# Kernel tuning notes

Hardware: AMD Instinct MI355X
Metric: run time of the kernel (lower is better)

## Reference

```python
import jax, jax.numpy as jnp
import numpy as np

N_HEAD = 16
D_MODEL = 1024
HEAD_DIM = D_MODEL // N_HEAD  # 64
LAMBDA_INIT = 0.8 - 0.6 * float(np.exp(-0.3 * 1))  # layer_depth = 1


def setup_inputs() -> dict:
    key = jax.random.key(0)
    ks = jax.random.split(key, 10)
    B, T, D = 1, 2048, D_MODEL
    std = 0.02
    return {
        "x": jax.random.normal(ks[0], (B, T, D), jnp.float32),
        "Wq": jax.random.normal(ks[1], (D, D), jnp.float32) * std,
        "Wk": jax.random.normal(ks[2], (D, D), jnp.float32) * std,
        "Wv": jax.random.normal(ks[3], (D, D), jnp.float32) * std,
        "Wproj": jax.random.normal(ks[4], (D, D), jnp.float32) * std,
        "lambda_q1": jax.random.normal(ks[5], (HEAD_DIM // 2,), jnp.float32) * 0.1,
        "lambda_k1": jax.random.normal(ks[6], (HEAD_DIM // 2,), jnp.float32) * 0.1,
        "lambda_q2": jax.random.normal(ks[7], (HEAD_DIM // 2,), jnp.float32) * 0.1,
        "lambda_k2": jax.random.normal(ks[8], (HEAD_DIM // 2,), jnp.float32) * 0.1,
    }


def _rms_norm(x):
    # F.rms_norm with no weight: x / sqrt(mean(x^2) + eps)
    eps = jnp.finfo(x.dtype).eps
    return x * jax.lax.rsqrt(jnp.mean(jnp.square(x), axis=-1, keepdims=True) + eps)


def _rotary_cos_sin(T, dim, base=10000.0):
    inv_freq = 1.0 / (base ** (jnp.arange(0, dim, 2, dtype=jnp.float32) / dim))
    freqs = jnp.outer(jnp.arange(T, dtype=jnp.float32), inv_freq)  # [T, dim/2]
    return jnp.cos(freqs), jnp.sin(freqs)


def _apply_rotary(x, cos, sin):
    # x: [B, T, 2, H, hd]; cos/sin: [T, hd/2] broadcast over (group, head)
    d = x.shape[-1] // 2
    c = cos[None, :, None, None, :]
    s = sin[None, :, None, None, :]
    x1, x2 = x[..., :d], x[..., d:]
    return jnp.concatenate([x1 * c + x2 * s, -x1 * s + x2 * c], axis=-1)


def _causal_attn(q, k, v, scale):
    # q,k: [B, T, H, hd]; v: [B, T, H, dv] -> [B, T, H, dv]
    T = q.shape[1]
    scores = jnp.einsum("bthd,bshd->bhts", q, k) * scale  # [B,H,T,T]
    mask = jnp.tril(jnp.ones((T, T), dtype=bool))
    scores = jnp.where(mask, scores, -jnp.inf)
    w = jax.nn.softmax(scores, axis=-1)
    return jnp.einsum("bhts,bshd->bthd", w, v)


def reference(x, Wq, Wk, Wv, Wproj, lambda_q1, lambda_k1, lambda_q2, lambda_k2):
    B, T, D = x.shape
    nh, hd = N_HEAD, HEAD_DIM
    q = (x @ Wq.T).reshape(B, T, 2, nh // 2, hd)
    k = (x @ Wk.T).reshape(B, T, 2, nh // 2, hd)
    v = (x @ Wv.T).reshape(B, T, nh // 2, 2 * hd)

    q, k = _rms_norm(q), _rms_norm(k)
    cos, sin = _rotary_cos_sin(T, hd)
    q, k = _apply_rotary(q, cos, sin), _apply_rotary(k, cos, sin)

    q1, q2 = q[:, :, 0], q[:, :, 1]
    k1, k2 = k[:, :, 0], k[:, :, 1]

    scale = 1.0 / jnp.sqrt(jnp.asarray(hd, x.dtype))
    y1 = _causal_attn(q1, k1, v, scale)  # [B,T,nh/2,2*hd]
    y2 = _causal_attn(q2, k2, v, scale)

    lambda_1 = jnp.exp(jnp.sum(lambda_q1 * lambda_k1))
    lambda_2 = jnp.exp(jnp.sum(lambda_q2 * lambda_k2))
    lambda_full = lambda_1 - lambda_2 + LAMBDA_INIT

    y = (y1 - lambda_full * y2).reshape(B, T, D)
    return y @ Wproj.T
```

## Files before the change

kernel.cpp:

```cpp
#include <hip/hip_runtime.h>
#include <hip/hip_bf16.h>

typedef __attribute__((ext_vector_type(4))) float f32x4;
typedef __attribute__((ext_vector_type(8))) short bf16x8;
typedef unsigned short u16;
typedef unsigned int u32;

#define T_SEQ 2048
#define DMODEL 1024

__device__ __forceinline__ u16 f2bf(float f) {
    __hip_bfloat16 h = __float2bfloat16(f);
    return __builtin_bit_cast(unsigned short, h);
}
__device__ __forceinline__ u16 f2h(float f) {
    _Float16 h = (_Float16)f;
    return __builtin_bit_cast(unsigned short, h);
}
__device__ __forceinline__ float h2f(u16 b) {
    return (float)__builtin_bit_cast(_Float16, b);
}

typedef const void __attribute__((address_space(1))) gvoid_t;
typedef void __attribute__((address_space(3))) lvoid_t;
__device__ __forceinline__ void gload16(const void* g, void* l) {
    __builtin_amdgcn_global_load_lds((gvoid_t*)g, (lvoid_t*)l, 16, 0, 0);
}

__device__ __forceinline__ void cast4(const float* __restrict__ s,
                                      u16* __restrict__ d, int u) {
    int i = u * 4;
    float4 v = *(const float4*)(s + i);
    ushort4 o;
    o.x = f2bf(v.x); o.y = f2bf(v.y); o.z = f2bf(v.z); o.w = f2bf(v.w);
    *(ushort4*)(d + i) = o;
}

__global__ __launch_bounds__(256) void prep(const float* __restrict__ x,
                                            const float* __restrict__ Wq,
                                            const float* __restrict__ Wk,
                                            const float* __restrict__ Wv,
                                            const float* __restrict__ Wp,
                                            u16* __restrict__ x_bf, u16* __restrict__ wq_bf,
                                            u16* __restrict__ wk_bf, u16* __restrict__ wv_bf,
                                            u16* __restrict__ wp_bf,
                                            float* __restrict__ cosT, float* __restrict__ sinT,
                                            const float* __restrict__ lq1, const float* __restrict__ lk1,
                                            const float* __restrict__ lq2, const float* __restrict__ lk2,
                                            float* __restrict__ lam) {
    int b = blockIdx.x;
    if (b < 6144) {
        int u = b * 256 + threadIdx.x;
        if (u < 524288)       cast4(x,  x_bf,  u);
        else if (u < 786432)  cast4(Wq, wq_bf, u - 524288);
        else if (u < 1048576) cast4(Wk, wk_bf, u - 786432);
        else if (u < 1310720) cast4(Wv, wv_bf, u - 1048576);
        else                  cast4(Wp, wp_bf, u - 1310720);
    } else if (b < 6400) {
        int i = (b - 6144) * 256 + threadIdx.x;
        int t = i >> 5, j = i & 31;
        float inv = powf(10000.0f, -(float)j * (1.0f / 32.0f));
        float fr = (float)t * inv;
        cosT[i] = cosf(fr);
        sinT[i] = sinf(fr);
    } else if (threadIdx.x == 0) {
        float s1 = 0.f, s2 = 0.f;
        for (int i = 0; i < 32; ++i) { s1 += lq1[i] * lk1[i]; s2 += lq2[i] * lk2[i]; }
        *lam = expf(s1) - expf(s2) + 0.35550906759096928f;
    }
}

__device__ __forceinline__ void gemm_main64(const u16* __restrict__ A,
                                            const u16* __restrict__ B,
                                            int m0, int n0, int K,
                                            u16* lA, u16* lB, f32x4 acc[2][4]) {
    const int tid = threadIdx.x;
    const int lane = tid & 63;
    const int wid = tid >> 6;
    const int wr = (wid >> 1) * 32;
    const int wc = (wid & 1) * 64;
    const int fr = lane & 15;
    const int kc = lane >> 4;
    const char* Ab = (const char*)A;
    const char* Bb = (const char*)B;
    const int rowbytes = K * 2;

    for (int k0 = 0; k0 < K; k0 += 64) {
#pragma unroll
        for (int i = 0; i < 2; ++i) {
            int seg = i * 256 + tid;
            int row = seg >> 3, cb = (seg & 7) * 16;
            gload16(Ab + (size_t)(m0 + row) * rowbytes + k0 * 2 + (cb ^ ((row & 7) << 4)),
                    (char*)lA + seg * 16);
        }
#pragma unroll
        for (int i = 0; i < 4; ++i) {
            int seg = i * 256 + tid;
            int row = seg >> 3, cb = (seg & 7) * 16;
            gload16(Bb + (size_t)(n0 + row) * rowbytes + k0 * 2 + (cb ^ ((row & 7) << 4)),
                    (char*)lB + seg * 16);
        }
        __syncthreads();
        bf16x8 a[2][2], b[4][2];
#pragma unroll
        for (int m = 0; m < 2; ++m)
#pragma unroll
            for (int kh = 0; kh < 2; ++kh) {
                int row = wr + m * 16 + fr;
                a[m][kh] = *(const bf16x8*)((char*)lA + row * 128 +
                                            ((kh * 64 + kc * 16) ^ ((row & 7) << 4)));
            }
#pragma unroll
        for (int n = 0; n < 4; ++n)
#pragma unroll
            for (int kh = 0; kh < 2; ++kh) {
                int row = wc + n * 16 + fr;
                b[n][kh] = *(const bf16x8*)((char*)lB + row * 128 +
                                            ((kh * 64 + kc * 16) ^ ((row & 7) << 4)));
            }
#pragma unroll
        for (int m = 0; m < 2; ++m)
#pragma unroll
            for (int n = 0; n < 4; ++n)
#pragma unroll
                for (int kh = 0; kh < 2; ++kh)
                    acc[m][n] = __builtin_amdgcn_mfma_f32_16x16x32_bf16(a[m][kh], b[n][kh],
                                                                        acc[m][n], 0, 0, 0);
        __syncthreads();
    }
}

__global__ __launch_bounds__(256) void gemm_qkv(const u16* __restrict__ A,
                                                const u16* __restrict__ wq,
                                                const u16* __restrict__ wk,
                                                const u16* __restrict__ wv,
                                                const float* __restrict__ cosT,
                                                const float* __restrict__ sinT,
                                                u16* __restrict__ q_bf,
                                                u16* __restrict__ k_bf,
                                                u16* __restrict__ vT) {
    __shared__ __align__(16) u16 lA[64 * 64];
    __shared__ __align__(16) u16 lB[128 * 64];
    const int nt = blockIdx.x;
    const int which = nt >> 3;
    const u16* B = (which == 0) ? wq : (which == 1) ? wk : wv;
    const int m0 = blockIdx.y * 64;
    const int n0 = (nt & 7) * 128;

    f32x4 acc[2][4] = {};
    gemm_main64(A, B, m0, n0, 1024, lA, lB, acc);

    const int lane = threadIdx.x & 63;
    const int wid = threadIdx.x >> 6;
    const int wr = (wid >> 1) * 32;
    const int wc = (wid & 1) * 64;
    const int fr = lane & 15;
    const int rr = (lane >> 4) * 4;

    if (which == 2) {
#pragma unroll
        for (int m = 0; m < 2; ++m) {
            int t0 = m0 + wr + m * 16 + rr;
#pragma unroll
            for (int n = 0; n < 4; ++n) {
                int cb = n0 + wc + n * 16 + fr;
                ushort4 w;
                w.x = f2bf(acc[m][n][0]);
                w.y = f2bf(acc[m][n][1]);
                w.z = f2bf(acc[m][n][2]);
                w.w = f2bf(acc[m][n][3]);
                *(ushort4*)(vT + (size_t)cb * T_SEQ + t0) = w;
            }
        }
        return;
    }

    const float oscale = (which == 0) ? 0.18033688011112042f : 1.0f;
    const int cb = n0 + wc;
    const int plane = ((cb >> 9) << 3) | ((cb >> 6) & 7);
    u16* dstp = ((which == 0) ? q_bf : k_bf) + (size_t)plane * T_SEQ * 64;
#pragma unroll
    for (int m = 0; m < 2; ++m)
#pragma unroll
        for (int r = 0; r < 4; ++r) {
            int t = m0 + wr + m * 16 + rr + r;
            float s2 = 0.f;
#pragma unroll
            for (int n = 0; n < 4; ++n) { float a = acc[m][n][r]; s2 += a * a; }
            s2 += __shfl_xor(s2, 1); s2 += __shfl_xor(s2, 2);
            s2 += __shfl_xor(s2, 4); s2 += __shfl_xor(s2, 8);
            float inv = rsqrtf(s2 * (1.0f / 64.0f) + 1.1920929e-7f);
#pragma unroll
            for (int n = 0; n < 4; ++n) {
                float a = acc[m][n][r] * inv;
                float p_ = acc[m][n ^ 2][r] * inv;
                int jj = ((n & 1) << 4) + fr;
                float c = cosT[t * 32 + jj], sn = sinT[t * 32 + jj];
                float ov = (n < 2) ? (a * c + p_ * sn) : (a * c - p_ * sn);
                dstp[(size_t)t * 64 + n * 16 + fr] = f2bf(ov * oscale);
            }
        }
}

__global__ __launch_bounds__(256) void gemm_proj(const u16* __restrict__ A,
                                                 const u16* __restrict__ B,
                                                 float* __restrict__ C) {
    __shared__ __align__(16) u16 lA[64 * 64];
    __shared__ __align__(16) u16 lB[128 * 64];
    const int m0 = blockIdx.y * 64;
    const int n0 = blockIdx.x * 128;
    f32x4 acc[2][4] = {};
    gemm_main64(A, B, m0, n0, 1024, lA, lB, acc);
    const int lane = threadIdx.x & 63;
    const int wid = threadIdx.x >> 6;
    const int wr = (wid >> 1) * 32;
    const int wc = (wid & 1) * 64;
    const int fr = lane & 15;
    const int rr = (lane >> 4) * 4;
#pragma unroll
    for (int m = 0; m < 2; ++m)
#pragma unroll
        for (int n = 0; n < 4; ++n)
#pragma unroll
            for (int r = 0; r < 4; ++r)
                C[(size_t)(m0 + wr + m * 16 + rr + r) * 1024 + (n0 + wc + n * 16 + fr)] =
                    acc[m][n][r];
}

__global__ __launch_bounds__(256, 6) void attn_kernel(const u16* __restrict__ q_bf,
                                                      const u16* __restrict__ k_bf,
                                                      const u16* __restrict__ vT_bf,
                                                      u16* __restrict__ Oc,
                                                      float2* __restrict__ ml) {
    __shared__ __align__(16) u16 lK[2][32 * 64];
    __shared__ __align__(16) u16 lV[2][64 * 64];

    const int tid = threadIdx.x, lane = tid & 63, wid = tid >> 6;
    const int bid = blockIdx.x;
    const int plane = bid & 15;
    const int u = bid >> 4;
    int qt, chunk;
    if (u < 32)      { qt = 31 - (u >> 2);              chunk = u & 3; }
    else if (u < 56) { int w = u - 32; qt = 23 - w / 3; chunk = w % 3; }
    else if (u < 72) { int w = u - 56; qt = 15 - (w >> 1); chunk = w & 1; }
    else             { qt = 7 - (u - 72);               chunk = 0; }
    const int ntot = 2 * qt + 2;
    const int tb = chunk * 16;
    const int te = min(tb + 16, ntot);
    const int q0 = qt * 64;
    const int h = plane & 7;

    const u16* qp = q_bf + (size_t)plane * T_SEQ * 64;
    const char* kp = (const char*)(k_bf + (size_t)plane * T_SEQ * 64);
    const char* vp = (const char*)(vT_bf + (size_t)h * 128 * T_SEQ);
    const int fr = lane & 15, kc = lane >> 4;
    const int qrow = q0 + wid * 16 + fr;

    bf16x8 aq[2];
#pragma unroll
    for (int kq = 0; kq < 2; ++kq)
        aq[kq] = *(const bf16x8*)(qp + (size_t)qrow * 64 + kq * 32 + kc * 8);

    f32x4 o[8] = {};
    float mi_l = -1e30f, li_l = 0.f;
    const int srcA = fr + ((kc & 1) << 5);
    const int srcB = srcA + 16;
    const bool hi = kc >= 2;

    auto stage = [&](int b, int t) {
        int s0 = t << 5;
        {
            int row = tid >> 3, cp = (tid & 7) * 16;
            gload16(kp + (size_t)(s0 + row) * 128 + (cp ^ ((row & 7) << 4)),
                    (char*)lK[b] + tid * 16);
        }
#pragma unroll
        for (int i = 0; i < 2; ++i) {
            int c = i * 256 + tid;
            int row = c >> 3, cb = (c & 7) * 16;
            int cbs = cb ^ ((row & 7) << 4);
            int d = row * 2 + (cbs >> 6);
            int kk = (cbs & 63) >> 1;
            gload16(vp + (size_t)d * (T_SEQ * 2) + (size_t)(s0 + kk) * 2,
                    (char*)lV[b] + c * 16);
        }
    };

    auto compute = [&](const char* lKb, const char* lVb, int s0, bool diag) {
        f32x4 sacc[2] = {};
        __builtin_amdgcn_s_setprio(1);
#pragma unroll
        for (int kq = 0; kq < 2; ++kq)
#pragma unroll
            for (int n = 0; n < 2; ++n) {
                int row = n * 16 + fr;
                bf16x8 bk = *(const bf16x8*)(lKb + row * 128 +
                                             ((kq * 64 + kc * 16) ^ ((row & 7) << 4)));
                sacc[n] = __builtin_amdgcn_mfma_f32_16x16x32_bf16(bk, aq[kq], sacc[n], 0, 0, 0);
            }
        __builtin_amdgcn_s_setprio(0);

        if (diag) {
#pragma unroll
            for (int n = 0; n < 2; ++n)
#pragma unroll
                for (int r = 0; r < 4; ++r)
                    if (s0 + n * 16 + kc * 4 + r > qrow) sacc[n][r] = -1e30f;
        }
        float rmax = -1e30f;
#pragma unroll
        for (int n = 0; n < 2; ++n)
#pragma unroll
            for (int r = 0; r < 4; ++r)
                rmax = fmaxf(rmax, sacc[n][r]);
        rmax = fmaxf(rmax, __shfl_xor(rmax, 16));
        rmax = fmaxf(rmax, __shfl_xor(rmax, 32));

        bool raise = rmax > mi_l + 8.0f;
        float f = raise ? __builtin_exp2f(mi_l - rmax) : 1.0f;
        if (raise) mi_l = rmax;

        float rs = 0.f;
#pragma unroll
        for (int n = 0; n < 2; ++n)
#pragma unroll
            for (int r = 0; r < 4; ++r) {
                float p = __builtin_exp2f(sacc[n][r] - mi_l);
                sacc[n][r] = p;
                rs += p;
            }
        rs += __shfl_xor(rs, 16);
        rs += __shfl_xor(rs, 32);
        li_l = li_l * f + rs;

        if (__any(raise)) {
#pragma unroll
            for (int n8 = 0; n8 < 8; ++n8)
#pragma unroll
                for (int r = 0; r < 4; ++r) o[n8][r] *= f;
        }

        u32 w32[2][2];
#pragma unroll
        for (int n = 0; n < 2; ++n)
#pragma unroll
            for (int w = 0; w < 2; ++w) {
                u32 rpk;
                asm("v_cvt_pk_bf16_f32 %0, %1, %2"
                    : "=v"(rpk) : "v"(sacc[n][2 * w]), "v"(sacc[n][2 * w + 1]));
                w32[n][w] = rpk;
            }

        u32 a0 = (u32)__shfl((int)w32[0][0], srcA);
        u32 a1 = (u32)__shfl((int)w32[0][1], srcA);
        u32 a2 = (u32)__shfl((int)w32[0][0], srcB);
        u32 a3 = (u32)__shfl((int)w32[0][1], srcB);
        u32 b0 = (u32)__shfl((int)w32[1][0], srcA);
        u32 b1 = (u32)__shfl((int)w32[1][1], srcA);
        u32 b2 = (u32)__shfl((int)w32[1][0], srcB);
        u32 b3 = (u32)__shfl((int)w32[1][1], srcB);
        union { u32 u4[4]; bf16x8 v; } ap;
        ap.u4[0] = hi ? b0 : a0;
        ap.u4[1] = hi ? b1 : a1;
        ap.u4[2] = hi ? b2 : a2;
        ap.u4[3] = hi ? b3 : a3;

        __builtin_amdgcn_s_setprio(1);
#pragma unroll
        for (int n8 = 0; n8 < 8; ++n8) {
            int d = n8 * 16 + fr;
            int row = d >> 1;
            int colb = (d & 1) * 64 + kc * 16;
            bf16x8 bv = *(const bf16x8*)(lVb + row * 128 + (colb ^ ((row & 7) << 4)));
            o[n8] = __builtin_amdgcn_mfma_f32_16x16x32_bf16(bv, ap.v, o[n8], 0, 0, 0);
        }
        __builtin_amdgcn_s_setprio(0);
    };

    stage(0, tb);
    for (int t = tb; t < te; ++t) {
        int ib = (t - tb) & 1;
        if (t + 1 < te) {
            stage(ib ^ 1, t + 1);
            asm volatile("s_waitcnt vmcnt(3)" ::: "memory");
        } else {
            asm volatile("s_waitcnt vmcnt(0)" ::: "memory");
        }
        __builtin_amdgcn_sched_barrier(0);
        __builtin_amdgcn_s_barrier();
        __builtin_amdgcn_sched_barrier(0);
        compute((const char*)lK[ib], (const char*)lV[ib], t << 5, t >= ntot - 2);
        __builtin_amdgcn_s_barrier();
    }

    const float inv_l = 1.0f / li_l;
    u16* Ob = Oc + ((size_t)(plane * 4 + chunk) * T_SEQ + qrow) * 128;
#pragma unroll
    for (int n8 = 0; n8 < 8; ++n8) {
        ushort4 w;
        w.x = f2h(o[n8][0] * inv_l);
        w.y = f2h(o[n8][1] * inv_l);
        w.z = f2h(o[n8][2] * inv_l);
        w.w = f2h(o[n8][3] * inv_l);
        *(ushort4*)(Ob + n8 * 16 + kc * 4) = w;
    }
    if (kc == 0)
        ml[(size_t)(plane * 4 + chunk) * T_SEQ + qrow] = make_float2(mi_l, li_l);
}

__global__ __launch_bounds__(256) void merge_kernel(const u16* __restrict__ Oc,
                                                    const float2* __restrict__ ml,
                                                    const float* __restrict__ lamp,
                                                    u16* __restrict__ yc) {
    int uu = blockIdx.x * 256 + threadIdx.x;
    int t = uu >> 8, rem = uu & 255, h = rem >> 5, d4 = (rem & 31) * 4;
    int qt = t >> 6;
    int nc = (qt + 8) >> 3;
    float lamv = *lamp;
    float yv[2][4];
#pragma unroll
    for (int v = 0; v < 2; ++v) {
        int plane = v * 8 + h;
        float2 m_l[4];
        float M = -1e30f;
#pragma unroll
        for (int c = 0; c < 4; ++c)
            if (c < nc) {
                m_l[c] = ml[(size_t)(plane * 4 + c) * T_SEQ + t];
                M = fmaxf(M, m_l[c].x);
            }
        float den = 0.f, a0 = 0.f, a1 = 0.f, a2 = 0.f, a3 = 0.f;
#pragma unroll
        for (int c = 0; c < 4; ++c)
            if (c < nc) {
                float w = __builtin_exp2f(m_l[c].x - M) * m_l[c].y;
                den += w;
                ushort4 ov = *(const ushort4*)(Oc +
                    ((size_t)(plane * 4 + c) * T_SEQ + t) * 128 + d4);
                a0 += w * h2f(ov.x);
                a1 += w * h2f(ov.y);
                a2 += w * h2f(ov.z);
                a3 += w * h2f(ov.w);
            }
        float inv = 1.0f / den;
        yv[v][0] = a0 * inv; yv[v][1] = a1 * inv;
        yv[v][2] = a2 * inv; yv[v][3] = a3 * inv;
    }
    ushort4 o;
    o.x = f2bf(yv[0][0] - lamv * yv[1][0]);
    o.y = f2bf(yv[0][1] - lamv * yv[1][1]);
    o.z = f2bf(yv[0][2] - lamv * yv[1][2]);
    o.w = f2bf(yv[0][3] - lamv * yv[1][3]);
    *(ushort4*)(yc + (size_t)t * 1024 + h * 128 + d4) = o;
}

extern "C" void kernel_launch(void* const* d_in, const int* in_sizes, int n_in,
                              void* d_out, int out_size, void* d_ws, size_t ws_size,
                              hipStream_t stream) {
    const float* x   = (const float*)d_in[0];
    const float* Wq  = (const float*)d_in[1];
    const float* Wk  = (const float*)d_in[2];
    const float* Wv  = (const float*)d_in[3];
    const float* Wp  = (const float*)d_in[4];
    const float* lq1 = (const float*)d_in[5];
    const float* lk1 = (const float*)d_in[6];
    const float* lq2 = (const float*)d_in[7];
    const float* lk2 = (const float*)d_in[8];
    float* out = (float*)d_out;

    char* ws = (char*)d_ws;
    u16*    x_bf  = (u16*)(ws);
    u16*    wq_bf = (u16*)(ws + (4ull << 20));
    u16*    wk_bf = (u16*)(ws + (6ull << 20));
    u16*    wv_bf = (u16*)(ws + (8ull << 20));
    u16*    wp_bf = (u16*)(ws + (10ull << 20));
    u16*    vT_bf = (u16*)(ws + (12ull << 20));
    u16*    q_bf  = (u16*)(ws + (16ull << 20));
    u16*    k_bf  = (u16*)(ws + (20ull << 20));
    u16*    Oc    = (u16*)(ws + (24ull << 20));
    float2* ml    = (float2*)(ws + (56ull << 20));
    u16*    yc_bf = (u16*)(ws + (57ull << 20));
    float*  cosT  = (float*)(ws + (61ull << 20));
    float*  sinT  = (float*)(ws + (61ull << 20) + (256ull << 10));
    float*  lam   = (float*)(ws + (61ull << 20) + (512ull << 10));

    prep<<<6401, 256, 0, stream>>>(x, Wq, Wk, Wv, Wp,
                                   x_bf, wq_bf, wk_bf, wv_bf, wp_bf,
                                   cosT, sinT, lq1, lk1, lq2, lk2, lam);

    gemm_qkv<<<dim3(24, 32), 256, 0, stream>>>(x_bf, wq_bf, wk_bf, wv_bf,
                                               cosT, sinT, q_bf, k_bf, vT_bf);

    attn_kernel<<<1280, 256, 0, stream>>>(q_bf, k_bf, vT_bf, Oc, ml);

    merge_kernel<<<2048, 256, 0, stream>>>(Oc, ml, lam, yc_bf);

    gemm_proj<<<dim3(8, 32), 256, 0, stream>>>(yc_bf, wp_bf, out);
}
```

Measured before the change: 93.44 us.

## Double-buffer LDS tiles in shared GEMM main loop to overlap loads

The shared GEMM mainloop used by the QKV and projection kernels now keeps two LDS buffers. It issues the next K-slice's global-to-LDS loads before computing on the current one, waiting with a partial vmcnt so only the older loads must finish. This is meant to hide global memory latency behind the MFMA work. In exchange it doubles the LDS per block, which can reduce occupancy, and it relies on hand-placed waitcnt and barriers whose counts must match the number of loads issued.

```diff
diff --git a/kernel.cpp b/kernel.cpp
--- a/kernel.cpp
+++ b/kernel.cpp
@@ -84,30 +84,49 @@
     const char* Ab = (const char*)A;
     const char* Bb = (const char*)B;
     const int rowbytes = K * 2;
-
-    for (int k0 = 0; k0 < K; k0 += 64) {
+    const int S = K >> 6;
+
+    auto stage = [&](int s, int buf) {
+        char* la = (char*)lA + buf * 8192;
+        char* lb = (char*)lB + buf * 16384;
 #pragma unroll
         for (int i = 0; i < 2; ++i) {
             int seg = i * 256 + tid;
             int row = seg >> 3, cb = (seg & 7) * 16;
-            gload16(Ab + (size_t)(m0 + row) * rowbytes + k0 * 2 + (cb ^ ((row & 7) << 4)),
-                    (char*)lA + seg * 16);
+            gload16(Ab + (size_t)(m0 + row) * rowbytes + s * 128 + (cb ^ ((row & 7) << 4)),
+                    la + seg * 16);
         }
 #pragma unroll
         for (int i = 0; i < 4; ++i) {
             int seg = i * 256 + tid;
             int row = seg >> 3, cb = (seg & 7) * 16;
-            gload16(Bb + (size_t)(n0 + row) * rowbytes + k0 * 2 + (cb ^ ((row & 7) << 4)),
-                    (char*)lB + seg * 16);
-        }
-        __syncthreads();
+            gload16(Bb + (size_t)(n0 + row) * rowbytes + s * 128 + (cb ^ ((row & 7) << 4)),
+                    lb + seg * 16);
+        }
+    };
+
+    stage(0, 0);
+    for (int s = 0; s < S; ++s) {
+        const int buf = s & 1;
+        if (s + 1 < S) {
+            stage(s + 1, buf ^ 1);
+            asm volatile("s_waitcnt vmcnt(6)" ::: "memory");
+        } else {
+            asm volatile("s_waitcnt vmcnt(0)" ::: "memory");
+        }
+        __builtin_amdgcn_sched_barrier(0);
+        __builtin_amdgcn_s_barrier();
+        __builtin_amdgcn_sched_barrier(0);
+
+        const char* la = (const char*)lA + buf * 8192;
+        const char* lb = (const char*)lB + buf * 16384;
         bf16x8 a[2][2], b[4][2];
 #pragma unroll
         for (int m = 0; m < 2; ++m)
 #pragma unroll
             for (int kh = 0; kh < 2; ++kh) {
                 int row = wr + m * 16 + fr;
-                a[m][kh] = *(const bf16x8*)((char*)lA + row * 128 +
+                a[m][kh] = *(const bf16x8*)(la + row * 128 +
                                             ((kh * 64 + kc * 16) ^ ((row & 7) << 4)));
             }
 #pragma unroll
@@ -115,7 +134,7 @@
 #pragma unroll
             for (int kh = 0; kh < 2; ++kh) {
                 int row = wc + n * 16 + fr;
-                b[n][kh] = *(const bf16x8*)((char*)lB + row * 128 +
+                b[n][kh] = *(const bf16x8*)(lb + row * 128 +
                                             ((kh * 64 + kc * 16) ^ ((row & 7) << 4)));
             }
 #pragma unroll
@@ -126,7 +145,7 @@
                 for (int kh = 0; kh < 2; ++kh)
                     acc[m][n] = __builtin_amdgcn_mfma_f32_16x16x32_bf16(a[m][kh], b[n][kh],
                                                                         acc[m][n], 0, 0, 0);
-        __syncthreads();
+        __builtin_amdgcn_s_barrier();
     }
 }
 
@@ -139,8 +158,8 @@
                                                 u16* __restrict__ q_bf,
                                                 u16* __restrict__ k_bf,
                                                 u16* __restrict__ vT) {
-    __shared__ __align__(16) u16 lA[64 * 64];
-    __shared__ __align__(16) u16 lB[128 * 64];
+    __shared__ __align__(16) u16 lA[2 * 64 * 64];
+    __shared__ __align__(16) u16 lB[2 * 128 * 64];
     const int nt = blockIdx.x;
     const int which = nt >> 3;
     const u16* B = (which == 0) ? wq : (which == 1) ? wk : wv;
@@ -205,8 +224,8 @@
 __global__ __launch_bounds__(256) void gemm_proj(const u16* __restrict__ A,
                                                  const u16* __restrict__ B,
                                                  float* __restrict__ C) {
-    __shared__ __align__(16) u16 lA[64 * 64];
-    __shared__ __align__(16) u16 lB[128 * 64];
+    __shared__ __align__(16) u16 lA[2 * 64 * 64];
+    __shared__ __align__(16) u16 lB[2 * 128 * 64];
     const int m0 = blockIdx.y * 64;
     const int n0 = blockIdx.x * 128;
     f32x4 acc[2][4] = {};
```

Result: faster. 90.70 us (median of 3 runs) (-2.9%).
